# Performance work log

Hardware: AMD Instinct MI355X
Metric: run time of the kernel (lower is better)

The kernel has to match this reference:

```python
import jax, jax.numpy as jnp
import numpy as np

B, N = 50000, 32


def _make_spd(key, b, n):
    a = jax.random.normal(key, (b, n, n), dtype=jnp.float32)
    # a @ a^T / n + I  -> well-conditioned SPD batch
    return jnp.matmul(a, jnp.swapaxes(a, -1, -2)) / n + jnp.eye(n, dtype=jnp.float32)


def setup_inputs() -> dict:
    key = jax.random.key(0)
    kx, ky = jax.random.split(key)
    return {"x": _make_spd(kx, B, N), "y": _make_spd(ky, B, N)}


def _invsqrtm(m):
    # batched SPD inverse square root via eigendecomposition
    w, v = jnp.linalg.eigh(m)                      # w: [B,N], v: [B,N,N]
    inv_sqrt_w = 1.0 / jnp.sqrt(w)
    return jnp.matmul(v * inv_sqrt_w[..., None, :], jnp.swapaxes(v, -1, -2))


def reference(x, y):
    # affine-invariant Riemannian distance:
    # d(x, y) = || logm(y^{-1/2} x y^{-1/2}) ||_F, then mean over batch
    y_is = _invsqrtm(y)                            # [B,N,N]
    m = jnp.matmul(jnp.matmul(y_is, x), y_is)      # [B,N,N], SPD
    w = jnp.linalg.eigh(m)[0]                      # [B,N] eigenvalues > 0
    d = jnp.sqrt(jnp.sum(jnp.log(w) ** 2, axis=-1))  # [B]
    return d.mean()
```

## Files before the change

kernel.cpp:

```cpp
#include <hip/hip_runtime.h>
#include <math.h>

#define NMAT 50000
#define MPB 8
#define NBLK (NMAT / MPB)

__device__ __forceinline__ float frcp(float x)  { return __builtin_amdgcn_rcpf(x); }
__device__ __forceinline__ float frsq(float x)  { return __builtin_amdgcn_rsqf(x); }
__device__ __forceinline__ float fsqrt_(float x){ return __builtin_amdgcn_sqrtf(x); }

#define SCHED_FENCE() __builtin_amdgcn_sched_barrier(0)

#define DPP_ROR_ADD(x, ctrl) \
  ((x) + __int_as_float(__builtin_amdgcn_update_dpp(0, __float_as_int(x), (ctrl), 0xF, 0xF, false)))

__device__ __forceinline__ float red32(float x) {
  x = DPP_ROR_ADD(x, 0x121);
  x = DPP_ROR_ADD(x, 0x122);
  x = DPP_ROR_ADD(x, 0x124);
  x = DPP_ROR_ADD(x, 0x128);
  x += __shfl_xor(x, 16, 32);
  return x;
}

__device__ __forceinline__ float f4c(const float4& v, int e) {
  return e == 0 ? v.x : e == 1 ? v.y : e == 2 ? v.z : v.w;
}

__global__ __launch_bounds__(256, 2) void riem_batch(const float* __restrict__ X,
                                                     const float* __restrict__ Y,
                                                     float* __restrict__ partial) {
  const int tid = threadIdx.x;
  const int c   = tid & 31;
  const int hw  = tid >> 5;
  const long mat = (long)blockIdx.x * MPB + hw;
  const float* Yp = Y + mat * 1024;
  const float* Xp = X + mat * 1024;

  __shared__ __align__(16) float Lb[MPB][1024];
  __shared__ __align__(16) float vb[MPB][32];
  __shared__ __align__(16) float qb[MPB][32];
  __shared__ __align__(16) float sb[MPB][64];
  __shared__ float psum[MPB];

  float* Lh = Lb[hw];
  float* vh = vb[hw];
  float* qh = qb[hw];
  float* sh = sb[hw];

  float m[32];
#pragma unroll
  for (int i = 0; i < 32; ++i) m[i] = Yp[i * 32 + c];

  float dc = 1.0f;
#pragma unroll
  for (int j = 0; j < 32; ++j) {
    float piv  = __shfl(m[j], j, 32);
    float rinv = frcp(piv);
    if (c == j) dc = piv;
    Lh[j * 32 + c] = m[j] * rinv;
    float mj = m[j];
#pragma unroll
    for (int g = 0; g < 8; ++g) {
      if (4 * g + 3 <= j) continue;
      float4 L4 = *(const float4*)(Lh + j * 32 + 4 * g);
#pragma unroll
      for (int e = 0; e < 4; ++e) {
        int i = 4 * g + e;
        if (i > j) m[i] = fmaf(-f4c(L4, e), mj, m[i]);
      }
    }
    SCHED_FENCE();
  }
  float dsv = frsq(dc);

  float x[32];
#pragma unroll
  for (int i = 0; i < 32; ++i) x[i] = Xp[i * 32 + c];
#pragma unroll
  for (int k = 0; k < 31; ++k) {
    float xk = x[k];
#pragma unroll
    for (int g = 0; g < 8; ++g) {
      if (4 * g + 3 <= k) continue;
      float4 L4 = *(const float4*)(Lh + k * 32 + 4 * g);
#pragma unroll
      for (int e = 0; e < 4; ++e) {
        int i = 4 * g + e;
        if (i > k) x[i] = fmaf(-f4c(L4, e), xk, x[i]);
      }
    }
    SCHED_FENCE();
  }

#pragma unroll
  for (int s = 16; s >= 1; s >>= 1) {
    const bool up = (c & s) != 0;
#pragma unroll
    for (int i = 0; i < 32; ++i) {
      if (i & s) continue;
      const int h2 = i | s;
      float send = up ? x[i] : x[h2];
      float rec  = __shfl_xor(send, s, 32);
      x[i]  = up ? rec : x[i];
      x[h2] = up ? x[h2] : rec;
    }
  }

#pragma unroll
  for (int k = 0; k < 31; ++k) {
    float xk = x[k];
#pragma unroll
    for (int g = 0; g < 8; ++g) {
      if (4 * g + 3 <= k) continue;
      float4 L4 = *(const float4*)(Lh + k * 32 + 4 * g);
#pragma unroll
      for (int e = 0; e < 4; ++e) {
        int i = 4 * g + e;
        if (i > k) x[i] = fmaf(-f4c(L4, e), xk, x[i]);
      }
    }
    SCHED_FENCE();
  }

  vh[c] = dsv;
#pragma unroll
  for (int g = 0; g < 8; ++g) {
    float4 D4 = *(const float4*)(vh + 4 * g);
#pragma unroll
    for (int e = 0; e < 4; ++e) x[4 * g + e] *= f4c(D4, e) * dsv;
  }

  float e2max = 0.0f, dminv = 1e30f, dmaxv = -1e30f;
#pragma unroll
  for (int k = 0; k < 30; ++k) {
    float colv = x[k];
    float dkk  = __shfl(x[k], k, 32);
    dminv = fminf(dminv, dkk); dmaxv = fmaxf(dmaxv, dkk);
    float sq    = (c > k) ? colv * colv : 0.0f;
    float sigma = red32(sq);
    float akk1  = __shfl(x[k], k + 1, 32);
    e2max = fmaxf(e2max, sigma);
    sh[k] = dkk;
    sh[32 + k] = sigma;
    float nrm   = fsqrt_(sigma);
    float alpha = (akk1 >= 0.0f) ? -nrm : nrm;
    float denom = fmaf(-alpha, akk1, sigma);
    float tau   = frcp(fmaxf(denom, 1e-35f));
    float v     = (c == k + 1) ? (akk1 - alpha) : ((c > k + 1) ? colv : 0.0f);
    vh[c] = v;
    float acc = 0.0f;
#pragma unroll
    for (int g = 0; g < 8; ++g) {
      if (4 * g + 3 <= k) continue;
      float4 V4 = *(const float4*)(vh + 4 * g);
#pragma unroll
      for (int e = 0; e < 4; ++e) {
        int j = 4 * g + e;
        if (j > k) acc = fmaf(x[j], f4c(V4, e), acc);
      }
    }
    float p = tau * acc;
    float K = 0.5f * tau * red32(v * p);
    float q = fmaf(-K, v, p);
    qh[c] = q;
#pragma unroll
    for (int g = 0; g < 8; ++g) {
      if (4 * g + 3 <= k) continue;
      float4 V4 = *(const float4*)(vh + 4 * g);
      float4 Q4 = *(const float4*)(qh + 4 * g);
#pragma unroll
      for (int e = 0; e < 4; ++e) {
        int j = 4 * g + e;
        if (j > k) x[j] = fmaf(-v, f4c(Q4, e), fmaf(-q, f4c(V4, e), x[j]));
      }
    }
    SCHED_FENCE();
  }
  {
    float d30 = __shfl(x[30], 30, 32);
    float d31 = __shfl(x[31], 31, 32);
    float el  = __shfl(x[30], 31, 32);
    float e30 = el * el;
    sh[30] = d30; sh[31] = d31; sh[62] = e30;
    e2max = fmaxf(e2max, e30);
    dminv = fminf(dminv, fminf(d30, d31));
    dmaxv = fmaxf(dmaxv, fmaxf(d30, d31));
  }

  float d[32], e2[31];
#pragma unroll
  for (int g = 0; g < 8; ++g) {
    float4 D4 = *(const float4*)(sh + 4 * g);
    d[4 * g + 0] = D4.x; d[4 * g + 1] = D4.y;
    d[4 * g + 2] = D4.z; d[4 * g + 3] = D4.w;
  }
#pragma unroll
  for (int g = 0; g < 8; ++g) {
    float4 E4 = *(const float4*)(sh + 32 + 4 * g);
    e2[4 * g + 0] = E4.x;
    if (4 * g + 1 < 31) e2[4 * g + 1] = E4.y;
    if (4 * g + 2 < 31) e2[4 * g + 2] = E4.z;
    if (4 * g + 3 < 31) e2[4 * g + 3] = E4.w;
  }

  float er = 2.0f * fsqrt_(e2max);
  float lo = fmaxf(dminv - er, 1e-3f);
  float hi = dmaxv + er;

  for (int it = 0; it < 15; ++it) {
    float mid = 0.5f * (lo + hi);
    float qq  = d[0] - mid;
    int cnt = (int)(__float_as_uint(qq) >> 31);
#pragma unroll
    for (int i = 1; i < 32; ++i) {
      qq = (d[i] - mid) - e2[i - 1] * frcp(qq);
      cnt += (int)(__float_as_uint(qq) >> 31);
    }
    bool le = (cnt <= c);
    lo = le ? mid : lo;
    hi = le ? hi : mid;
  }

  float lam = 0.5f * (lo + hi);
  float lg  = __logf(lam);
  float s   = red32(lg * lg);
  float db  = fsqrt_(s);

  if (c == 0) psum[hw] = db;
  __syncthreads();
  if (tid == 0) {
    float t = 0.0f;
#pragma unroll
    for (int i = 0; i < MPB; ++i) t += psum[i];
    partial[blockIdx.x] = t;
  }
}

__global__ __launch_bounds__(256) void riem_finish(const float* __restrict__ partial,
                                                   float* __restrict__ out) {
  float acc = 0.0f;
  for (int i = threadIdx.x; i < NBLK; i += 256) acc += partial[i];
  acc += __shfl_xor(acc, 1);
  acc += __shfl_xor(acc, 2);
  acc += __shfl_xor(acc, 4);
  acc += __shfl_xor(acc, 8);
  acc += __shfl_xor(acc, 16);
  acc += __shfl_xor(acc, 32);
  __shared__ float ps[4];
  if ((threadIdx.x & 63) == 0) ps[threadIdx.x >> 6] = acc;
  __syncthreads();
  if (threadIdx.x == 0)
    out[0] = (ps[0] + ps[1] + ps[2] + ps[3]) * (1.0f / (float)NMAT);
}

extern "C" void kernel_launch(void* const* d_in, const int* in_sizes, int n_in,
                              void* d_out, int out_size, void* d_ws, size_t ws_size,
                              hipStream_t stream) {
  const float* x = (const float*)d_in[0];
  const float* y = (const float*)d_in[1];
  float* out  = (float*)d_out;
  float* part = (float*)d_ws;
  riem_batch<<<NBLK, 256, 0, stream>>>(x, y, part);
  riem_finish<<<1, 256, 0, stream>>>(part, out);
}
```

Before: 804.8 us.

## Use packed FP32 FMAs across factorization and tridiagonalization, cut bisection iterations

Stores the per-lane matrix columns as two-wide float vectors so the Cholesky, triangular solves, scaling and Householder updates can issue packed FMA instructions, roughly halving VALU instruction count. The Sturm-count bisection now precomputes d-mid with packed subtracts, fuses the update into one fma, and runs 12 iterations instead of 15. Fewer bisection steps loosen the eigenvalue bracket and may cost accuracy in the log-eigenvalue distance. Packed operands can also raise register pressure.

```diff
diff --git a/kernel.cpp b/kernel.cpp
--- a/kernel.cpp
+++ b/kernel.cpp
@@ -4,6 +4,13 @@
 #define NMAT 50000
 #define MPB 8
 #define NBLK (NMAT / MPB)
+
+typedef __attribute__((ext_vector_type(2))) float f32x2;
+#define EL(a, i) (a[(i) >> 1][(i) & 1])
+
+__device__ __forceinline__ f32x2 pkfma(f32x2 a, f32x2 b, f32x2 c) {
+  return __builtin_elementwise_fma(a, b, c);
+}
 
 __device__ __forceinline__ float frcp(float x)  { return __builtin_amdgcn_rcpf(x); }
 __device__ __forceinline__ float frsq(float x)  { return __builtin_amdgcn_rsqf(x); }
@@ -48,46 +55,58 @@
   float* qh = qb[hw];
   float* sh = sb[hw];
 
-  float m[32];
-#pragma unroll
-  for (int i = 0; i < 32; ++i) m[i] = Yp[i * 32 + c];
+  f32x2 m2[16];
+#pragma unroll
+  for (int i = 0; i < 32; ++i) EL(m2, i) = Yp[i * 32 + c];
 
   float dc = 1.0f;
 #pragma unroll
   for (int j = 0; j < 32; ++j) {
-    float piv  = __shfl(m[j], j, 32);
+    float mjv  = EL(m2, j);
+    float piv  = __shfl(mjv, j, 32);
     float rinv = frcp(piv);
     if (c == j) dc = piv;
-    Lh[j * 32 + c] = m[j] * rinv;
-    float mj = m[j];
+    Lh[j * 32 + c] = mjv * rinv;
+    f32x2 mj2 = { mjv, mjv };
 #pragma unroll
     for (int g = 0; g < 8; ++g) {
       if (4 * g + 3 <= j) continue;
       float4 L4 = *(const float4*)(Lh + j * 32 + 4 * g);
-#pragma unroll
-      for (int e = 0; e < 4; ++e) {
-        int i = 4 * g + e;
-        if (i > j) m[i] = fmaf(-f4c(L4, e), mj, m[i]);
+      if (4 * g + 1 > j) {
+        f32x2 l = { L4.x, L4.y };
+        m2[2 * g] = pkfma(-l, mj2, m2[2 * g]);
+      }
+      if (4 * g + 3 > j) {
+        f32x2 l = { L4.z, L4.w };
+        m2[2 * g + 1] = pkfma(-l, mj2, m2[2 * g + 1]);
       }
     }
     SCHED_FENCE();
   }
   float dsv = frsq(dc);
 
-  float x[32];
-#pragma unroll
-  for (int i = 0; i < 32; ++i) x[i] = Xp[i * 32 + c];
+  f32x2 x2[16];
+#pragma unroll
+  for (int i = 0; i < 32; ++i) EL(x2, i) = Xp[i * 32 + c];
 #pragma unroll
   for (int k = 0; k < 31; ++k) {
-    float xk = x[k];
+    float xk = EL(x2, k);
+    f32x2 xk2 = { xk, xk };
 #pragma unroll
     for (int g = 0; g < 8; ++g) {
       if (4 * g + 3 <= k) continue;
       float4 L4 = *(const float4*)(Lh + k * 32 + 4 * g);
-#pragma unroll
-      for (int e = 0; e < 4; ++e) {
-        int i = 4 * g + e;
-        if (i > k) x[i] = fmaf(-f4c(L4, e), xk, x[i]);
+      if (4 * g > k) {
+        f32x2 l = { L4.x, L4.y };
+        x2[2 * g] = pkfma(-l, xk2, x2[2 * g]);
+      } else if (4 * g == k) {
+        EL(x2, 4 * g + 1) = fmaf(-L4.y, xk, EL(x2, 4 * g + 1));
+      }
+      if (4 * g + 2 > k) {
+        f32x2 l = { L4.z, L4.w };
+        x2[2 * g + 1] = pkfma(-l, xk2, x2[2 * g + 1]);
+      } else if (4 * g + 2 == k) {
+        EL(x2, 4 * g + 3) = fmaf(-L4.w, xk, EL(x2, 4 * g + 3));
       }
     }
     SCHED_FENCE();
@@ -100,46 +119,59 @@
     for (int i = 0; i < 32; ++i) {
       if (i & s) continue;
       const int h2 = i | s;
-      float send = up ? x[i] : x[h2];
+      float send = up ? EL(x2, i) : EL(x2, h2);
       float rec  = __shfl_xor(send, s, 32);
-      x[i]  = up ? rec : x[i];
-      x[h2] = up ? x[h2] : rec;
+      EL(x2, i)  = up ? rec : EL(x2, i);
+      EL(x2, h2) = up ? EL(x2, h2) : rec;
     }
   }
 
 #pragma unroll
   for (int k = 0; k < 31; ++k) {
-    float xk = x[k];
+    float xk = EL(x2, k);
+    f32x2 xk2 = { xk, xk };
 #pragma unroll
     for (int g = 0; g < 8; ++g) {
       if (4 * g + 3 <= k) continue;
       float4 L4 = *(const float4*)(Lh + k * 32 + 4 * g);
-#pragma unroll
-      for (int e = 0; e < 4; ++e) {
-        int i = 4 * g + e;
-        if (i > k) x[i] = fmaf(-f4c(L4, e), xk, x[i]);
+      if (4 * g > k) {
+        f32x2 l = { L4.x, L4.y };
+        x2[2 * g] = pkfma(-l, xk2, x2[2 * g]);
+      } else if (4 * g == k) {
+        EL(x2, 4 * g + 1) = fmaf(-L4.y, xk, EL(x2, 4 * g + 1));
+      }
+      if (4 * g + 2 > k) {
+        f32x2 l = { L4.z, L4.w };
+        x2[2 * g + 1] = pkfma(-l, xk2, x2[2 * g + 1]);
+      } else if (4 * g + 2 == k) {
+        EL(x2, 4 * g + 3) = fmaf(-L4.w, xk, EL(x2, 4 * g + 3));
       }
     }
     SCHED_FENCE();
   }
 
   vh[c] = dsv;
-#pragma unroll
-  for (int g = 0; g < 8; ++g) {
-    float4 D4 = *(const float4*)(vh + 4 * g);
-#pragma unroll
-    for (int e = 0; e < 4; ++e) x[4 * g + e] *= f4c(D4, e) * dsv;
+  {
+    f32x2 dsv2 = { dsv, dsv };
+#pragma unroll
+    for (int g = 0; g < 8; ++g) {
+      float4 D4 = *(const float4*)(vh + 4 * g);
+      f32x2 a = { D4.x, D4.y };
+      f32x2 b = { D4.z, D4.w };
+      x2[2 * g]     = x2[2 * g]     * a * dsv2;
+      x2[2 * g + 1] = x2[2 * g + 1] * b * dsv2;
+    }
   }
 
   float e2max = 0.0f, dminv = 1e30f, dmaxv = -1e30f;
 #pragma unroll
   for (int k = 0; k < 30; ++k) {
-    float colv = x[k];
-    float dkk  = __shfl(x[k], k, 32);
+    float colv = EL(x2, k);
+    float dkk  = __shfl(colv, k, 32);
     dminv = fminf(dminv, dkk); dmaxv = fmaxf(dmaxv, dkk);
     float sq    = (c > k) ? colv * colv : 0.0f;
     float sigma = red32(sq);
-    float akk1  = __shfl(x[k], k + 1, 32);
+    float akk1  = __shfl(colv, k + 1, 32);
     e2max = fmaxf(e2max, sigma);
     sh[k] = dkk;
     sh[32 + k] = sigma;
@@ -149,38 +181,51 @@
     float tau   = frcp(fmaxf(denom, 1e-35f));
     float v     = (c == k + 1) ? (akk1 - alpha) : ((c > k + 1) ? colv : 0.0f);
     vh[c] = v;
-    float acc = 0.0f;
+    f32x2 acc2 = { 0.0f, 0.0f };
 #pragma unroll
     for (int g = 0; g < 8; ++g) {
       if (4 * g + 3 <= k) continue;
       float4 V4 = *(const float4*)(vh + 4 * g);
-#pragma unroll
-      for (int e = 0; e < 4; ++e) {
-        int j = 4 * g + e;
-        if (j > k) acc = fmaf(x[j], f4c(V4, e), acc);
-      }
-    }
+      if (4 * g + 1 > k) {
+        f32x2 vv = { V4.x, V4.y };
+        acc2 = pkfma(x2[2 * g], vv, acc2);
+      }
+      if (4 * g + 3 > k) {
+        f32x2 vv = { V4.z, V4.w };
+        acc2 = pkfma(x2[2 * g + 1], vv, acc2);
+      }
+    }
+    float acc = acc2.x + acc2.y;
     float p = tau * acc;
     float K = 0.5f * tau * red32(v * p);
     float q = fmaf(-K, v, p);
     qh[c] = q;
+    f32x2 vl = { v, v };
+    f32x2 ql = { q, q };
 #pragma unroll
     for (int g = 0; g < 8; ++g) {
       if (4 * g + 3 <= k) continue;
       float4 V4 = *(const float4*)(vh + 4 * g);
       float4 Q4 = *(const float4*)(qh + 4 * g);
-#pragma unroll
-      for (int e = 0; e < 4; ++e) {
-        int j = 4 * g + e;
-        if (j > k) x[j] = fmaf(-v, f4c(Q4, e), fmaf(-q, f4c(V4, e), x[j]));
+      if (4 * g + 1 > k) {
+        f32x2 qv = { Q4.x, Q4.y };
+        f32x2 vv = { V4.x, V4.y };
+        f32x2 t = pkfma(-vl, qv, x2[2 * g]);
+        x2[2 * g] = pkfma(-ql, vv, t);
+      }
+      if (4 * g + 3 > k) {
+        f32x2 qv = { Q4.z, Q4.w };
+        f32x2 vv = { V4.z, V4.w };
+        f32x2 t = pkfma(-vl, qv, x2[2 * g + 1]);
+        x2[2 * g + 1] = pkfma(-ql, vv, t);
       }
     }
     SCHED_FENCE();
   }
   {
-    float d30 = __shfl(x[30], 30, 32);
-    float d31 = __shfl(x[31], 31, 32);
-    float el  = __shfl(x[30], 31, 32);
+    float d30 = __shfl(EL(x2, 30), 30, 32);
+    float d31 = __shfl(EL(x2, 31), 31, 32);
+    float el  = __shfl(EL(x2, 30), 31, 32);
     float e30 = el * el;
     sh[30] = d30; sh[31] = d31; sh[62] = e30;
     e2max = fmaxf(e2max, e30);
@@ -188,12 +233,14 @@
     dmaxv = fmaxf(dmaxv, fmaxf(d30, d31));
   }
 
-  float d[32], e2[31];
+  f32x2 d2[16];
+  float e2[31];
 #pragma unroll
   for (int g = 0; g < 8; ++g) {
     float4 D4 = *(const float4*)(sh + 4 * g);
-    d[4 * g + 0] = D4.x; d[4 * g + 1] = D4.y;
-    d[4 * g + 2] = D4.z; d[4 * g + 3] = D4.w;
+    f32x2 a = { D4.x, D4.y };
+    f32x2 b = { D4.z, D4.w };
+    d2[2 * g] = a; d2[2 * g + 1] = b;
   }
 #pragma unroll
   for (int g = 0; g < 8; ++g) {
@@ -208,13 +255,17 @@
   float lo = fmaxf(dminv - er, 1e-3f);
   float hi = dmaxv + er;
 
-  for (int it = 0; it < 15; ++it) {
+  for (int it = 0; it < 12; ++it) {
     float mid = 0.5f * (lo + hi);
-    float qq  = d[0] - mid;
+    f32x2 mid2 = { mid, mid };
+    f32x2 dm2[16];
+#pragma unroll
+    for (int pp = 0; pp < 16; ++pp) dm2[pp] = d2[pp] - mid2;
+    float qq = EL(dm2, 0);
     int cnt = (int)(__float_as_uint(qq) >> 31);
 #pragma unroll
     for (int i = 1; i < 32; ++i) {
-      qq = (d[i] - mid) - e2[i - 1] * frcp(qq);
+      qq = fmaf(-e2[i - 1], frcp(qq), EL(dm2, i));
       cnt += (int)(__float_as_uint(qq) >> 31);
     }
     bool le = (cnt <= c);
```

After: 703.7 us. 1.14x faster.
